# Kernel tuning notes

Hardware: AMD Instinct MI355X
Metric: run time of the kernel (lower is better)

The kernel has to match this reference:

```python
import jax, jax.numpy as jnp
import numpy as np

H = 16          # num_heads
LN_EPS = 1e-5   # torch LayerNorm default


def _ln(x, g, b):
    m = jnp.mean(x, axis=-1, keepdims=True)
    v = jnp.var(x, axis=-1, keepdims=True)
    return (x - m) * jax.lax.rsqrt(v + LN_EPS) * g + b


def _cross_attn(xq, xkv, wq, wk, wv, wp, bp):
    B, N, C = xq.shape
    d = C // H
    scale = d ** -0.5
    q = (xq @ wq).reshape(B, N, H, d).transpose(0, 2, 1, 3)   # bhnd
    k = (xkv @ wk).reshape(B, N, H, d).transpose(0, 2, 1, 3)
    v = (xkv @ wv).reshape(B, N, H, d).transpose(0, 2, 1, 3)
    attn = jax.nn.softmax(jnp.einsum('bhnd,bhmd->bhnm', q, k) * scale, axis=-1)
    out = jnp.einsum('bhnm,bhmd->bhnd', attn, v).transpose(0, 2, 1, 3).reshape(B, N, C)
    return out @ wp + bp


def setup_inputs() -> dict:
    key = jax.random.key(0)
    ks = jax.random.split(key, 16)
    B, N, C, Hid = 8, 1024, 1024, 4096
    s = 0.02
    inp = {
        'x_1': jax.random.normal(ks[0], (B, N, C), jnp.float32),
        'x_2': jax.random.normal(ks[1], (B, N, C), jnp.float32),
        'x_3': jax.random.normal(ks[2], (B, N, C), jnp.float32),
        'ln11_g': jnp.ones((C,), jnp.float32), 'ln11_b': jnp.zeros((C,), jnp.float32),
        'ln12_g': jnp.ones((C,), jnp.float32), 'ln12_b': jnp.zeros((C,), jnp.float32),
        'ln21_g': jnp.ones((C,), jnp.float32), 'ln21_b': jnp.zeros((C,), jnp.float32),
        'ln23_g': jnp.ones((C,), jnp.float32), 'ln23_b': jnp.zeros((C,), jnp.float32),
        'ln2_g': jnp.ones((C,), jnp.float32), 'ln2_b': jnp.zeros((C,), jnp.float32),
        'a1_wq': s * jax.random.normal(ks[3], (C, C), jnp.float32),
        'a1_wk': s * jax.random.normal(ks[4], (C, C), jnp.float32),
        'a1_wv': s * jax.random.normal(ks[5], (C, C), jnp.float32),
        'a1_wp': s * jax.random.normal(ks[6], (C, C), jnp.float32),
        'a1_bp': jnp.zeros((C,), jnp.float32),
        'a2_wq': s * jax.random.normal(ks[7], (C, C), jnp.float32),
        'a2_wk': s * jax.random.normal(ks[8], (C, C), jnp.float32),
        'a2_wv': s * jax.random.normal(ks[9], (C, C), jnp.float32),
        'a2_wp': s * jax.random.normal(ks[10], (C, C), jnp.float32),
        'a2_bp': jnp.zeros((C,), jnp.float32),
        'fc1_w': s * jax.random.normal(ks[11], (C, Hid), jnp.float32),
        'fc1_b': jnp.zeros((Hid,), jnp.float32),
        'fc2_w': s * jax.random.normal(ks[12], (Hid, C), jnp.float32),
        'fc2_b': jnp.zeros((C,), jnp.float32),
    }
    return inp


def reference(x_1, x_2, x_3,
              ln11_g, ln11_b, ln12_g, ln12_b, ln21_g, ln21_b, ln23_g, ln23_b,
              ln2_g, ln2_b,
              a1_wq, a1_wk, a1_wv, a1_wp, a1_bp,
              a2_wq, a2_wk, a2_wv, a2_wp, a2_bp,
              fc1_w, fc1_b, fc2_w, fc2_b):
    # dual cross-attention branches + residual (drop_path/dropout are identity at p=0)
    br1 = _cross_attn(_ln(x_1, ln11_g, ln11_b), _ln(x_2, ln12_g, ln12_b),
                      a1_wq, a1_wk, a1_wv, a1_wp, a1_bp)
    br2 = _cross_attn(_ln(x_1, ln21_g, ln21_b), _ln(x_3, ln23_g, ln23_b),
                      a2_wq, a2_wk, a2_wv, a2_wp, a2_bp)
    x = x_1 + br1 + br2
    # MLP block
    h = jax.nn.gelu(_ln(x, ln2_g, ln2_b) @ fc1_w + fc1_b, approximate=False)
    x = x + (h @ fc2_w + fc2_b)
    return x
```

## Files before the change

### kernel.cpp

```cpp
#include <hip/hip_runtime.h>
#include <hip/hip_bf16.h>
#include <cstdint>

typedef unsigned short u16;
typedef __bf16 v8bf __attribute__((ext_vector_type(8)));
typedef short v4s __attribute__((ext_vector_type(4)));
typedef float v4f __attribute__((ext_vector_type(4)));

__device__ __forceinline__ u16 f2bf(float f) {
  union { float f; uint32_t u; } v; v.f = f;
  return (u16)((v.u + 0x7fffu + ((v.u >> 16) & 1u)) >> 16);
}

#define GLL16(gsrc, ldst) \
  __builtin_amdgcn_global_load_lds((__attribute__((address_space(1))) void*)(gsrc), \
      (__attribute__((address_space(3))) void*)(ldst), 16, 0, 0)

__global__ __launch_bounds__(256) void ln_kernel(
    const float* __restrict__ x, const float* __restrict__ g, const float* __restrict__ bt,
    u16* __restrict__ out)
{
  int row = blockIdx.x, tid = threadIdx.x;
  const float4* xr = (const float4*)(x + (size_t)row * 1024);
  float4 v = xr[tid];
  float s = v.x + v.y + v.z + v.w;
  float ss = v.x*v.x + v.y*v.y + v.z*v.z + v.w*v.w;
  for (int d = 1; d < 64; d <<= 1) { s += __shfl_xor(s, d); ss += __shfl_xor(ss, d); }
  __shared__ float red[8];
  int wv = tid >> 6, lane = tid & 63;
  if (lane == 0) { red[wv] = s; red[4 + wv] = ss; }
  __syncthreads();
  s  = red[0] + red[1] + red[2] + red[3];
  ss = red[4] + red[5] + red[6] + red[7];
  float mean = s * (1.f/1024.f);
  float var  = ss * (1.f/1024.f) - mean*mean;
  float rs = rsqrtf(var + 1e-5f);
  float4 gv = ((const float4*)g)[tid];
  float4 bv = ((const float4*)bt)[tid];
  ushort4 o;
  o.x = f2bf((v.x-mean)*rs*gv.x + bv.x);
  o.y = f2bf((v.y-mean)*rs*gv.y + bv.y);
  o.z = f2bf((v.z-mean)*rs*gv.z + bv.z);
  o.w = f2bf((v.w-mean)*rs*gv.w + bv.w);
  ((ushort4*)out)[(size_t)row*256 + tid] = o;
}

__global__ __launch_bounds__(256) void transpose_cast(
    const float* __restrict__ W, u16* __restrict__ WT, int K, int N)
{
  __shared__ float t[32][33];
  int tiles_n = N >> 5;
  int bn = blockIdx.x % tiles_n, bk = blockIdx.x / tiles_n;
  int tx = threadIdx.x & 31, ty = threadIdx.x >> 5;
  #pragma unroll
  for (int j = 0; j < 4; ++j)
    t[ty + j*8][tx] = W[(size_t)(bk*32 + ty + j*8) * N + bn*32 + tx];
  __syncthreads();
  #pragma unroll
  for (int j = 0; j < 4; ++j)
    WT[(size_t)(bn*32 + ty + j*8) * K + bk*32 + tx] = f2bf(t[tx][ty + j*8]);
}

template<int EPI>
__global__ __launch_bounds__(256, 2) void gemm_bf16(
    const u16* __restrict__ A, const u16* __restrict__ Bt, void* __restrict__ Cout,
    const float* __restrict__ bias, const float* __restrict__ r1, const float* __restrict__ r2,
    int M, int N, int K)
{
  int tiles_n = N >> 7;
  int bm = blockIdx.x / tiles_n, bn = blockIdx.x % tiles_n;
  int tid = threadIdx.x, wv = tid >> 6, lane = tid & 63, quad = lane >> 4, lc = lane & 15;
  int wm = wv & 1, wn = wv >> 1;

  __shared__ __align__(16) u16 lds_[16384];
  char* la = (char*)lds_;
  char* lb = (char*)lds_ + 16384;

  v4f acc[4][4] = {};

  for (int kt = 0; kt < K; kt += 64) {
    __syncthreads();
    #pragma unroll
    for (int c0 = 0; c0 < 4; ++c0) {
      int chunk = wv*4 + c0;
      int off = chunk*1024 + lane*16;
      int row = off >> 7;
      int sc  = (off >> 4) & 7;
      int lg  = sc ^ (row & 7);
      const u16* ga = A  + (size_t)(bm*128 + row) * K + kt + lg*8;
      GLL16(ga, la + chunk*1024);
      const u16* gb = Bt + (size_t)(bn*128 + row) * K + kt + lg*8;
      GLL16(gb, lb + chunk*1024);
    }
    __syncthreads();

    #pragma unroll
    for (int kc = 0; kc < 2; ++kc) {
      v8bf af[4], bfr[4];
      #pragma unroll
      for (int r = 0; r < 4; ++r) {
        int row = wm*64 + r*16 + lc;
        int sc = (kc*4 + quad) ^ (row & 7);
        af[r] = *(const v8bf*)(la + row*128 + sc*16);
      }
      #pragma unroll
      for (int c = 0; c < 4; ++c) {
        int row = wn*64 + c*16 + lc;
        int sc = (kc*4 + quad) ^ (row & 7);
        bfr[c] = *(const v8bf*)(lb + row*128 + sc*16);
      }
      #pragma unroll
      for (int r = 0; r < 4; ++r)
        #pragma unroll
        for (int c = 0; c < 4; ++c)
          acc[r][c] = __builtin_amdgcn_mfma_f32_16x16x32_bf16(af[r], bfr[c], acc[r][c], 0, 0, 0);
    }
  }

  #pragma unroll
  for (int r = 0; r < 4; ++r) {
    int grow = bm*128 + wm*64 + r*16 + quad*4;
    #pragma unroll
    for (int c = 0; c < 4; ++c) {
      int gcol = bn*128 + wn*64 + c*16 + lc;
      if (EPI == 5) {
        ushort4 o;
        o.x = f2bf(acc[r][c][0]); o.y = f2bf(acc[r][c][1]);
        o.z = f2bf(acc[r][c][2]); o.w = f2bf(acc[r][c][3]);
        *(ushort4*)((u16*)Cout + (size_t)gcol * M + grow) = o;
        continue;
      }
      float bv = (EPI != 0) ? bias[gcol] : 0.f;
      #pragma unroll
      for (int i = 0; i < 4; ++i) {
        size_t idx = (size_t)(grow + i) * N + gcol;
        float v = acc[r][c][i] + bv;
        if (EPI == 0) {
          ((u16*)Cout)[idx] = f2bf(v);
        } else if (EPI == 1) {
          float ge = 0.5f * v * (1.f + erff(v * 0.70710678118654752f));
          ((u16*)Cout)[idx] = f2bf(ge);
        } else if (EPI == 2) {
          ((float*)Cout)[idx] = v;
        } else if (EPI == 3) {
          ((float*)Cout)[idx] = v + r1[idx] + r2[idx];
        } else {
          ((float*)Cout)[idx] = v + r1[idx];
        }
      }
    }
  }
}

__global__ __launch_bounds__(256, 2) void attn_kernel(
    const u16* __restrict__ Q, const u16* __restrict__ K, const u16* __restrict__ VT,
    u16* __restrict__ O)
{
  int bid = blockIdx.x;
  int qt = bid & 15, h = (bid >> 4) & 15, b = bid >> 8;
  int tid = threadIdx.x, wv = tid >> 6, lane = tid & 63, quad = lane >> 4, lc = lane & 15;

  __shared__ __align__(16) char lds_[32768];
  char* kt_l = lds_;
  char* vt_l = lds_ + 16384;

  const float scale = 0.125f;

  v8bf qf[2];
  {
    int qrow = qt*64 + wv*16 + lc;
    const u16* qp = Q + ((size_t)(b*1024 + qrow) * 1024 + h*64 + quad*8);
    qf[0] = *(const v8bf*)qp;
    qf[1] = *(const v8bf*)(qp + 32);
  }

  float m_i = -1e30f, l_i = 0.f;
  v4f oacc[4] = {};

  for (int it = 0; it < 8; ++it) {
    int kvb = it * 128;
    __syncthreads();
    #pragma unroll
    for (int c0 = 0; c0 < 4; ++c0) {
      int ch = wv*4 + c0;
      int off = ch*1024 + lane*16;
      {
        int row = off >> 7, sc = (off >> 4) & 7, lg = sc ^ (row & 7);
        const u16* g = K + (size_t)(b*1024 + kvb + row) * 1024 + h*64 + lg*8;
        GLL16(g, kt_l + ch*1024);
      }
      {
        int row = off >> 8, sc = (off >> 4) & 15, lg = sc ^ (row & 15);
        const u16* g = VT + (size_t)(h*64 + row) * 8192 + b*1024 + kvb + lg*8;
        GLL16(g, vt_l + ch*1024);
      }
    }
    __syncthreads();

    v4f s[8] = {};
    #pragma unroll
    for (int ct = 0; ct < 8; ++ct) {
      int row = ct*16 + lc;
      #pragma unroll
      for (int kc = 0; kc < 2; ++kc) {
        int sc = (kc*4 + quad) ^ (row & 7);
        v8bf kf = *(const v8bf*)(kt_l + row*128 + sc*16);
        s[ct] = __builtin_amdgcn_mfma_f32_16x16x32_bf16(kf, qf[kc], s[ct], 0, 0, 0);
      }
    }

    float mx = m_i;
    #pragma unroll
    for (int ct = 0; ct < 8; ++ct)
      #pragma unroll
      for (int i = 0; i < 4; ++i) mx = fmaxf(mx, s[ct][i] * scale);
    mx = fmaxf(mx, __shfl_xor(mx, 16));
    mx = fmaxf(mx, __shfl_xor(mx, 32));
    float alpha = __expf(m_i - mx);
    float rs = 0.f;
    #pragma unroll
    for (int ct = 0; ct < 8; ++ct)
      #pragma unroll
      for (int i = 0; i < 4; ++i) {
        float p = __expf(s[ct][i] * scale - mx);
        s[ct][i] = p;
        rs += p;
      }
    rs += __shfl_xor(rs, 16);
    rs += __shfl_xor(rs, 32);
    l_i = l_i * alpha + rs;
    m_i = mx;
    #pragma unroll
    for (int dt = 0; dt < 4; ++dt)
      #pragma unroll
      for (int i = 0; i < 4; ++i) oacc[dt][i] *= alpha;

    #pragma unroll
    for (int ct = 0; ct < 8; ++ct) {
      v4s pfrag;
      #pragma unroll
      for (int i = 0; i < 4; ++i) pfrag[i] = (short)f2bf(s[ct][i]);
      int lg = ct*2 + (quad >> 1);
      int ho = (quad & 1) * 8;
      #pragma unroll
      for (int dt = 0; dt < 4; ++dt) {
        int rowd = dt*16 + lc;
        int sc = lg ^ (rowd & 15);
        v4s vfrag = *(const v4s*)(vt_l + rowd*256 + sc*16 + ho);
        oacc[dt] = __builtin_amdgcn_mfma_f32_16x16x16bf16_1k(vfrag, pfrag, oacc[dt], 0, 0, 0);
      }
    }
  }

  __syncthreads();
  {
    char* base = kt_l + wv*2048;
    float inv = 1.f / l_i;
    #pragma unroll
    for (int dt = 0; dt < 4; ++dt) {
      ushort4 o;
      o.x = f2bf(oacc[dt][0]*inv); o.y = f2bf(oacc[dt][1]*inv);
      o.z = f2bf(oacc[dt][2]*inv); o.w = f2bf(oacc[dt][3]*inv);
      int lg = dt*2 + (quad >> 1);
      int sc = lg ^ (lc & 7);
      *(ushort4*)(base + lc*128 + sc*16 + (quad & 1)*8) = o;
    }
  }
  __syncthreads();
  {
    char* base = kt_l + wv*2048;
    #pragma unroll
    for (int rep = 0; rep < 2; ++rep) {
      int qr = rep*8 + (lane >> 3);
      int ch = lane & 7;
      int sc = ch ^ (qr & 7);
      uint4 d = *(const uint4*)(base + qr*128 + sc*16);
      *(uint4*)(O + (size_t)(b*1024 + qt*64 + wv*16 + qr) * 1024 + h*64 + ch*8) = d;
    }
  }
}

extern "C" void kernel_launch(void* const* d_in, const int* in_sizes, int n_in,
                              void* d_out, int out_size, void* d_ws, size_t ws_size,
                              hipStream_t stream)
{
  const float* x1    = (const float*)d_in[0];
  const float* x2    = (const float*)d_in[1];
  const float* x3    = (const float*)d_in[2];
  const float* ln11g = (const float*)d_in[3];
  const float* ln11b = (const float*)d_in[4];
  const float* ln12g = (const float*)d_in[5];
  const float* ln12b = (const float*)d_in[6];
  const float* ln21g = (const float*)d_in[7];
  const float* ln21b = (const float*)d_in[8];
  const float* ln23g = (const float*)d_in[9];
  const float* ln23b = (const float*)d_in[10];
  const float* ln2g  = (const float*)d_in[11];
  const float* ln2b  = (const float*)d_in[12];
  const float* a1wq  = (const float*)d_in[13];
  const float* a1wk  = (const float*)d_in[14];
  const float* a1wv  = (const float*)d_in[15];
  const float* a1wp  = (const float*)d_in[16];
  const float* a1bp  = (const float*)d_in[17];
  const float* a2wq  = (const float*)d_in[18];
  const float* a2wk  = (const float*)d_in[19];
  const float* a2wv  = (const float*)d_in[20];
  const float* a2wp  = (const float*)d_in[21];
  const float* a2bp  = (const float*)d_in[22];
  const float* fc1w  = (const float*)d_in[23];
  const float* fc1b  = (const float*)d_in[24];
  const float* fc2w  = (const float*)d_in[25];
  const float* fc2b  = (const float*)d_in[26];

  const int M = 8192, C = 1024, HID = 4096;
  char* ws = (char*)d_ws;
  u16* WT = (u16*)ws;
  #define SLOT(i) ((void*)(ws + ((size_t)8 << 20) + (size_t)(i) * ((size_t)16 << 20)))

  dim3 blk(256);
  const int gC  = (M/128) * (C/128);
  const int gH  = (M/128) * (HID/128);
  const int tCC = (C/32) * (C/32);

  ln_kernel<<<M, blk, 0, stream>>>(x1, ln11g, ln11b, (u16*)SLOT(0));
  ln_kernel<<<M, blk, 0, stream>>>(x2, ln12g, ln12b, (u16*)SLOT(1));

  transpose_cast<<<tCC, blk, 0, stream>>>(a1wq, WT, C, C);
  gemm_bf16<0><<<gC, blk, 0, stream>>>((u16*)SLOT(0), WT, SLOT(2), nullptr, nullptr, nullptr, M, C, C);
  transpose_cast<<<tCC, blk, 0, stream>>>(a1wk, WT, C, C);
  gemm_bf16<0><<<gC, blk, 0, stream>>>((u16*)SLOT(1), WT, SLOT(3), nullptr, nullptr, nullptr, M, C, C);
  transpose_cast<<<tCC, blk, 0, stream>>>(a1wv, WT, C, C);
  gemm_bf16<5><<<gC, blk, 0, stream>>>((u16*)SLOT(1), WT, SLOT(4), nullptr, nullptr, nullptr, M, C, C);

  attn_kernel<<<2048, blk, 0, stream>>>((u16*)SLOT(2), (u16*)SLOT(3), (u16*)SLOT(4), (u16*)SLOT(0));

  transpose_cast<<<tCC, blk, 0, stream>>>(a1wp, WT, C, C);
  gemm_bf16<2><<<gC, blk, 0, stream>>>((u16*)SLOT(0), WT, SLOT(5), a1bp, nullptr, nullptr, M, C, C);

  ln_kernel<<<M, blk, 0, stream>>>(x1, ln21g, ln21b, (u16*)SLOT(1));
  ln_kernel<<<M, blk, 0, stream>>>(x3, ln23g, ln23b, (u16*)SLOT(2));

  transpose_cast<<<tCC, blk, 0, stream>>>(a2wq, WT, C, C);
  gemm_bf16<0><<<gC, blk, 0, stream>>>((u16*)SLOT(1), WT, SLOT(3), nullptr, nullptr, nullptr, M, C, C);
  transpose_cast<<<tCC, blk, 0, stream>>>(a2wk, WT, C, C);
  gemm_bf16<0><<<gC, blk, 0, stream>>>((u16*)SLOT(2), WT, SLOT(4), nullptr, nullptr, nullptr, M, C, C);
  transpose_cast<<<tCC, blk, 0, stream>>>(a2wv, WT, C, C);
  gemm_bf16<5><<<gC, blk, 0, stream>>>((u16*)SLOT(2), WT, SLOT(0), nullptr, nullptr, nullptr, M, C, C);

  attn_kernel<<<2048, blk, 0, stream>>>((u16*)SLOT(3), (u16*)SLOT(4), (u16*)SLOT(0), (u16*)SLOT(1));

  transpose_cast<<<tCC, blk, 0, stream>>>(a2wp, WT, C, C);
  gemm_bf16<3><<<gC, blk, 0, stream>>>((u16*)SLOT(1), WT, SLOT(2), a2bp, x1, (const float*)SLOT(5), M, C, C);

  ln_kernel<<<M, blk, 0, stream>>>((const float*)SLOT(2), ln2g, ln2b, (u16*)SLOT(4));
  transpose_cast<<<(C/32)*(HID/32), blk, 0, stream>>>(fc1w, WT, C, HID);
  gemm_bf16<1><<<gH, blk, 0, stream>>>((u16*)SLOT(4), WT, SLOT(5), fc1b, nullptr, nullptr, M, HID, C);
  transpose_cast<<<(HID/32)*(C/32), blk, 0, stream>>>(fc2w, WT, HID, C);
  gemm_bf16<4><<<gC, blk, 0, stream>>>((u16*)SLOT(5), WT, d_out, fc2b, (const float*)SLOT(2), nullptr, M, C, HID);
  #undef SLOT
}
```

Before: 772.1 us.

## Batch prep, QKV GEMMs, and co-schedule attention with projection GEMM

```diff
diff --git a/kernel.cpp b/kernel.cpp
--- a/kernel.cpp
+++ b/kernel.cpp
@@ -11,10 +11,116 @@
   union { float f; uint32_t u; } v; v.f = f;
   return (u16)((v.u + 0x7fffu + ((v.u >> 16) & 1u)) >> 16);
 }
+__device__ __forceinline__ float bf2f(u16 u) {
+  union { uint32_t u; float f; } v; v.u = ((uint32_t)u) << 16; return v.f;
+}
 
 #define GLL16(gsrc, ldst) \
   __builtin_amdgcn_global_load_lds((__attribute__((address_space(1))) void*)(gsrc), \
       (__attribute__((address_space(3))) void*)(ldst), 16, 0, 0)
+
+#define TILE_MAP(blk, bm, bn) \
+  int bm = ((blk) & 7) * 8 + (((blk) >> 3) & 7); \
+  int bn = (blk) >> 6;
+
+__device__ __forceinline__ void gemm_core(
+    const u16* __restrict__ A, const u16* __restrict__ Bt, int K,
+    char* la, char* lb, int bm, int bn, int tid, v4f acc[4][4])
+{
+  int wv = tid >> 6, lane = tid & 63, quad = lane >> 4, lc = lane & 15;
+  int wm = wv & 1, wn = wv >> 1;
+  for (int kt = 0; kt < K; kt += 64) {
+    __syncthreads();
+    #pragma unroll
+    for (int c0 = 0; c0 < 4; ++c0) {
+      int chunk = wv*4 + c0;
+      int off = chunk*1024 + lane*16;
+      int row = off >> 7;
+      int sc  = (off >> 4) & 7;
+      int lg  = sc ^ (row & 7);
+      GLL16(A  + (size_t)(bm*128 + row) * K + kt + lg*8, la + chunk*1024);
+      GLL16(Bt + (size_t)(bn*128 + row) * K + kt + lg*8, lb + chunk*1024);
+    }
+    __syncthreads();
+    #pragma unroll
+    for (int kc = 0; kc < 2; ++kc) {
+      v8bf af[4], bfr[4];
+      #pragma unroll
+      for (int r = 0; r < 4; ++r) {
+        int row = wm*64 + r*16 + lc;
+        int sc = (kc*4 + quad) ^ (row & 7);
+        af[r] = *(const v8bf*)(la + row*128 + sc*16);
+      }
+      #pragma unroll
+      for (int c = 0; c < 4; ++c) {
+        int row = wn*64 + c*16 + lc;
+        int sc = (kc*4 + quad) ^ (row & 7);
+        bfr[c] = *(const v8bf*)(lb + row*128 + sc*16);
+      }
+      #pragma unroll
+      for (int r = 0; r < 4; ++r)
+        #pragma unroll
+        for (int c = 0; c < 4; ++c)
+          acc[r][c] = __builtin_amdgcn_mfma_f32_16x16x32_bf16(af[r], bfr[c], acc[r][c], 0, 0, 0);
+    }
+  }
+}
+
+struct TDesc { const float* W; u16* WT; int K, N, tstart; };
+struct PrepArgs {
+  TDesc d[10];
+  const float* lx[4]; const float* lg[4]; const float* lb_[4]; u16* lo[4];
+  int ts;
+};
+__global__ __launch_bounds__(256) void prep_kernel(PrepArgs P)
+{
+  __shared__ float sh[32*33];
+  int tid = threadIdx.x;
+  if ((int)blockIdx.x < P.ts) {
+    int bi = blockIdx.x;
+    int idx = 0;
+    #pragma unroll
+    for (int i = 1; i < 10; ++i) if (bi >= P.d[i].tstart) idx = i;
+    const float* W = P.d[idx].W;
+    u16* WT = P.d[idx].WT;
+    int K = P.d[idx].K, N = P.d[idx].N;
+    int loc = bi - P.d[idx].tstart;
+    int tiles_n = N >> 5;
+    int bn = loc % tiles_n, bk = loc / tiles_n;
+    int tx = tid & 31, ty = tid >> 5;
+    #pragma unroll
+    for (int j = 0; j < 4; ++j)
+      sh[(ty + j*8)*33 + tx] = W[(size_t)(bk*32 + ty + j*8) * N + bn*32 + tx];
+    __syncthreads();
+    #pragma unroll
+    for (int j = 0; j < 4; ++j)
+      WT[(size_t)(bn*32 + ty + j*8) * K + bk*32 + tx] = f2bf(sh[tx*33 + ty + j*8]);
+  } else {
+    int lid = blockIdx.x - P.ts;
+    int id = lid >> 13, row = lid & 8191;
+    const float4* xr = (const float4*)(P.lx[id] + (size_t)row * 1024);
+    float4 v = xr[tid];
+    float s = v.x + v.y + v.z + v.w;
+    float ss = v.x*v.x + v.y*v.y + v.z*v.z + v.w*v.w;
+    for (int d = 1; d < 64; d <<= 1) { s += __shfl_xor(s, d); ss += __shfl_xor(ss, d); }
+    int wv = tid >> 6, lane = tid & 63;
+    if (lane == 0) { sh[wv] = s; sh[4 + wv] = ss; }
+    __syncthreads();
+    s  = sh[0] + sh[1] + sh[2] + sh[3];
+    ss = sh[4] + sh[5] + sh[6] + sh[7];
+    float mean = s * (1.f/1024.f);
+    float var  = ss * (1.f/1024.f) - mean*mean;
+    float rs = rsqrtf(var + 1e-5f);
+    float4 gv = ((const float4*)P.lg[id])[tid];
+    float4 bv = ((const float4*)P.lb_[id])[tid];
+    ushort4 o;
+    o.x = f2bf((v.x-mean)*rs*gv.x + bv.x);
+    o.y = f2bf((v.y-mean)*rs*gv.y + bv.y);
+    o.z = f2bf((v.z-mean)*rs*gv.z + bv.z);
+    o.w = f2bf((v.w-mean)*rs*gv.w + bv.w);
+    ((ushort4*)P.lo[id])[(size_t)row*256 + tid] = o;
+  }
+}
 
 __global__ __launch_bounds__(256) void ln_kernel(
     const float* __restrict__ x, const float* __restrict__ g, const float* __restrict__ bt,
@@ -45,125 +151,47 @@
   ((ushort4*)out)[(size_t)row*256 + tid] = o;
 }
 
-__global__ __launch_bounds__(256) void transpose_cast(
-    const float* __restrict__ W, u16* __restrict__ WT, int K, int N)
-{
-  __shared__ float t[32][33];
-  int tiles_n = N >> 5;
-  int bn = blockIdx.x % tiles_n, bk = blockIdx.x / tiles_n;
-  int tx = threadIdx.x & 31, ty = threadIdx.x >> 5;
-  #pragma unroll
-  for (int j = 0; j < 4; ++j)
-    t[ty + j*8][tx] = W[(size_t)(bk*32 + ty + j*8) * N + bn*32 + tx];
-  __syncthreads();
-  #pragma unroll
-  for (int j = 0; j < 4; ++j)
-    WT[(size_t)(bn*32 + ty + j*8) * K + bk*32 + tx] = f2bf(t[tx][ty + j*8]);
-}
-
-template<int EPI>
-__global__ __launch_bounds__(256, 2) void gemm_bf16(
-    const u16* __restrict__ A, const u16* __restrict__ Bt, void* __restrict__ Cout,
-    const float* __restrict__ bias, const float* __restrict__ r1, const float* __restrict__ r2,
-    int M, int N, int K)
-{
-  int tiles_n = N >> 7;
-  int bm = blockIdx.x / tiles_n, bn = blockIdx.x % tiles_n;
+struct QkvArgs { const u16* A[3]; const u16* Bt[3]; u16* C[3]; };
+__global__ __launch_bounds__(256, 3) void gemm_qkv(QkvArgs P)
+{
+  int sub = blockIdx.x >> 9;
+  int local = blockIdx.x & 511;
+  TILE_MAP(local, bm, bn)
   int tid = threadIdx.x, wv = tid >> 6, lane = tid & 63, quad = lane >> 4, lc = lane & 15;
   int wm = wv & 1, wn = wv >> 1;
-
-  __shared__ __align__(16) u16 lds_[16384];
-  char* la = (char*)lds_;
-  char* lb = (char*)lds_ + 16384;
-
+  __shared__ __align__(16) char lds_[32768];
   v4f acc[4][4] = {};
-
-  for (int kt = 0; kt < K; kt += 64) {
-    __syncthreads();
-    #pragma unroll
-    for (int c0 = 0; c0 < 4; ++c0) {
-      int chunk = wv*4 + c0;
-      int off = chunk*1024 + lane*16;
-      int row = off >> 7;
-      int sc  = (off >> 4) & 7;
-      int lg  = sc ^ (row & 7);
-      const u16* ga = A  + (size_t)(bm*128 + row) * K + kt + lg*8;
-      GLL16(ga, la + chunk*1024);
-      const u16* gb = Bt + (size_t)(bn*128 + row) * K + kt + lg*8;
-      GLL16(gb, lb + chunk*1024);
-    }
-    __syncthreads();
-
-    #pragma unroll
-    for (int kc = 0; kc < 2; ++kc) {
-      v8bf af[4], bfr[4];
-      #pragma unroll
-      for (int r = 0; r < 4; ++r) {
-        int row = wm*64 + r*16 + lc;
-        int sc = (kc*4 + quad) ^ (row & 7);
-        af[r] = *(const v8bf*)(la + row*128 + sc*16);
-      }
-      #pragma unroll
-      for (int c = 0; c < 4; ++c) {
-        int row = wn*64 + c*16 + lc;
-        int sc = (kc*4 + quad) ^ (row & 7);
-        bfr[c] = *(const v8bf*)(lb + row*128 + sc*16);
-      }
-      #pragma unroll
-      for (int r = 0; r < 4; ++r)
-        #pragma unroll
-        for (int c = 0; c < 4; ++c)
-          acc[r][c] = __builtin_amdgcn_mfma_f32_16x16x32_bf16(af[r], bfr[c], acc[r][c], 0, 0, 0);
-    }
-  }
-
+  gemm_core(P.A[sub], P.Bt[sub], 1024, lds_, lds_ + 16384, bm, bn, tid, acc);
+
+  u16* Cout = P.C[sub];
   #pragma unroll
   for (int r = 0; r < 4; ++r) {
     int grow = bm*128 + wm*64 + r*16 + quad*4;
     #pragma unroll
     for (int c = 0; c < 4; ++c) {
       int gcol = bn*128 + wn*64 + c*16 + lc;
-      if (EPI == 5) {
+      if (sub == 2) {
         ushort4 o;
         o.x = f2bf(acc[r][c][0]); o.y = f2bf(acc[r][c][1]);
         o.z = f2bf(acc[r][c][2]); o.w = f2bf(acc[r][c][3]);
-        *(ushort4*)((u16*)Cout + (size_t)gcol * M + grow) = o;
-        continue;
-      }
-      float bv = (EPI != 0) ? bias[gcol] : 0.f;
-      #pragma unroll
-      for (int i = 0; i < 4; ++i) {
-        size_t idx = (size_t)(grow + i) * N + gcol;
-        float v = acc[r][c][i] + bv;
-        if (EPI == 0) {
-          ((u16*)Cout)[idx] = f2bf(v);
-        } else if (EPI == 1) {
-          float ge = 0.5f * v * (1.f + erff(v * 0.70710678118654752f));
-          ((u16*)Cout)[idx] = f2bf(ge);
-        } else if (EPI == 2) {
-          ((float*)Cout)[idx] = v;
-        } else if (EPI == 3) {
-          ((float*)Cout)[idx] = v + r1[idx] + r2[idx];
-        } else {
-          ((float*)Cout)[idx] = v + r1[idx];
-        }
-      }
-    }
-  }
-}
-
-__global__ __launch_bounds__(256, 2) void attn_kernel(
+        *(ushort4*)(Cout + (size_t)gcol * 8192 + grow) = o;
+      } else {
+        #pragma unroll
+        for (int i = 0; i < 4; ++i)
+          Cout[(size_t)(grow + i) * 1024 + gcol] = f2bf(acc[r][c][i]);
+      }
+    }
+  }
+}
+
+__device__ __forceinline__ void attn_body(
     const u16* __restrict__ Q, const u16* __restrict__ K, const u16* __restrict__ VT,
-    u16* __restrict__ O)
-{
-  int bid = blockIdx.x;
+    u16* __restrict__ O, int bid, int tid, char* lds_)
+{
   int qt = bid & 15, h = (bid >> 4) & 15, b = bid >> 8;
-  int tid = threadIdx.x, wv = tid >> 6, lane = tid & 63, quad = lane >> 4, lc = lane & 15;
-
-  __shared__ __align__(16) char lds_[32768];
+  int wv = tid >> 6, lane = tid & 63, quad = lane >> 4, lc = lane & 15;
   char* kt_l = lds_;
   char* vt_l = lds_ + 16384;
-
   const float scale = 0.125f;
 
   v8bf qf[2];
@@ -186,13 +214,11 @@
       int off = ch*1024 + lane*16;
       {
         int row = off >> 7, sc = (off >> 4) & 7, lg = sc ^ (row & 7);
-        const u16* g = K + (size_t)(b*1024 + kvb + row) * 1024 + h*64 + lg*8;
-        GLL16(g, kt_l + ch*1024);
+        GLL16(K + (size_t)(b*1024 + kvb + row) * 1024 + h*64 + lg*8, kt_l + ch*1024);
       }
       {
         int row = off >> 8, sc = (off >> 4) & 15, lg = sc ^ (row & 15);
-        const u16* g = VT + (size_t)(h*64 + row) * 8192 + b*1024 + kvb + lg*8;
-        GLL16(g, vt_l + ch*1024);
+        GLL16(VT + (size_t)(h*64 + row) * 8192 + b*1024 + kvb + lg*8, vt_l + ch*1024);
       }
     }
     __syncthreads();
@@ -276,6 +302,127 @@
       int sc = ch ^ (qr & 7);
       uint4 d = *(const uint4*)(base + qr*128 + sc*16);
       *(uint4*)(O + (size_t)(b*1024 + qt*64 + wv*16 + qr) * 1024 + h*64 + ch*8) = d;
+    }
+  }
+}
+
+__global__ __launch_bounds__(256, 4) void attn_kernel(
+    const u16* __restrict__ Q, const u16* __restrict__ K, const u16* __restrict__ VT,
+    u16* __restrict__ O)
+{
+  __shared__ __align__(16) char lds_[32768];
+  attn_body(Q, K, VT, O, blockIdx.x, threadIdx.x, lds_);
+}
+
+__global__ __launch_bounds__(256, 3) void attn_proj_kernel(
+    const u16* __restrict__ Q, const u16* __restrict__ K, const u16* __restrict__ VT,
+    u16* __restrict__ O,
+    const u16* __restrict__ GA, const u16* __restrict__ GBt,
+    const float* __restrict__ Gbias, u16* __restrict__ GC)
+{
+  __shared__ __align__(16) char lds_[32768];
+  int tid = threadIdx.x;
+  if ((int)blockIdx.x < 2048) {
+    attn_body(Q, K, VT, O, blockIdx.x, tid, lds_);
+  } else {
+    int local = blockIdx.x - 2048;
+    TILE_MAP(local, bm, bn)
+    int wv = tid >> 6, lane = tid & 63, quad = lane >> 4, lc = lane & 15;
+    int wm = wv & 1, wn = wv >> 1;
+    v4f acc[4][4] = {};
+    gemm_core(GA, GBt, 1024, lds_, lds_ + 16384, bm, bn, tid, acc);
+    #pragma unroll
+    for (int r = 0; r < 4; ++r) {
+      int grow = bm*128 + wm*64 + r*16 + quad*4;
+      #pragma unroll
+      for (int c = 0; c < 4; ++c) {
+        int gcol = bn*128 + wn*64 + c*16 + lc;
+        float bv = Gbias[gcol];
+        #pragma unroll
+        for (int i = 0; i < 4; ++i)
+          GC[(size_t)(grow + i) * 1024 + gcol] = f2bf(acc[r][c][i] + bv);
+      }
+    }
+  }
+}
+
+__global__ __launch_bounds__(256, 3) void gemm_projadd(
+    const u16* __restrict__ A, const u16* __restrict__ Bt,
+    const float* __restrict__ bias, const float* __restrict__ x1,
+    const u16* __restrict__ o1b, float* __restrict__ xsum)
+{
+  TILE_MAP((int)blockIdx.x, bm, bn)
+  int tid = threadIdx.x, wv = tid >> 6, lane = tid & 63, quad = lane >> 4, lc = lane & 15;
+  int wm = wv & 1, wn = wv >> 1;
+  __shared__ __align__(16) char lds_[32768];
+  v4f acc[4][4] = {};
+  gemm_core(A, Bt, 1024, lds_, lds_ + 16384, bm, bn, tid, acc);
+  #pragma unroll
+  for (int r = 0; r < 4; ++r) {
+    int grow = bm*128 + wm*64 + r*16 + quad*4;
+    #pragma unroll
+    for (int c = 0; c < 4; ++c) {
+      int gcol = bn*128 + wn*64 + c*16 + lc;
+      float bv = bias[gcol];
+      #pragma unroll
+      for (int i = 0; i < 4; ++i) {
+        size_t idx = (size_t)(grow + i) * 1024 + gcol;
+        xsum[idx] = acc[r][c][i] + bv + x1[idx] + bf2f(o1b[idx]);
+      }
+    }
+  }
+}
+
+__global__ __launch_bounds__(256, 3) void gemm_fc1(
+    const u16* __restrict__ A, const u16* __restrict__ Bt,
+    const float* __restrict__ bias, u16* __restrict__ C)
+{
+  TILE_MAP((int)blockIdx.x, bm, bn)
+  int tid = threadIdx.x, wv = tid >> 6, lane = tid & 63, quad = lane >> 4, lc = lane & 15;
+  int wm = wv & 1, wn = wv >> 1;
+  __shared__ __align__(16) char lds_[32768];
+  v4f acc[4][4] = {};
+  gemm_core(A, Bt, 1024, lds_, lds_ + 16384, bm, bn, tid, acc);
+  #pragma unroll
+  for (int r = 0; r < 4; ++r) {
+    int grow = bm*128 + wm*64 + r*16 + quad*4;
+    #pragma unroll
+    for (int c = 0; c < 4; ++c) {
+      int gcol = bn*128 + wn*64 + c*16 + lc;
+      float bv = bias[gcol];
+      #pragma unroll
+      for (int i = 0; i < 4; ++i) {
+        float v = acc[r][c][i] + bv;
+        float ge = 0.5f * v * (1.f + erff(v * 0.70710678118654752f));
+        C[(size_t)(grow + i) * 4096 + gcol] = f2bf(ge);
+      }
+    }
+  }
+}
+
+__global__ __launch_bounds__(256, 3) void gemm_fc2(
+    const u16* __restrict__ A, const u16* __restrict__ Bt,
+    const float* __restrict__ bias, const float* __restrict__ r1,
+    float* __restrict__ C)
+{
+  TILE_MAP((int)blockIdx.x, bm, bn)
+  int tid = threadIdx.x, wv = tid >> 6, lane = tid & 63, quad = lane >> 4, lc = lane & 15;
+  int wm = wv & 1, wn = wv >> 1;
+  __shared__ __align__(16) char lds_[32768];
+  v4f acc[4][4] = {};
+  gemm_core(A, Bt, 4096, lds_, lds_ + 16384, bm, bn, tid, acc);
+  #pragma unroll
+  for (int r = 0; r < 4; ++r) {
+    int grow = bm*128 + wm*64 + r*16 + quad*4;
+    #pragma unroll
+    for (int c = 0; c < 4; ++c) {
+      int gcol = bn*128 + wn*64 + c*16 + lc;
+      float bv = bias[gcol];
+      #pragma unroll
+      for (int i = 0; i < 4; ++i) {
+        size_t idx = (size_t)(grow + i) * 1024 + gcol;
+        C[idx] = acc[r][c][i] + bv + r1[idx];
+      }
     }
   }
 }
@@ -312,50 +459,64 @@
   const float* fc2w  = (const float*)d_in[25];
   const float* fc2b  = (const float*)d_in[26];
 
-  const int M = 8192, C = 1024, HID = 4096;
   char* ws = (char*)d_ws;
-  u16* WT = (u16*)ws;
-  #define SLOT(i) ((void*)(ws + ((size_t)8 << 20) + (size_t)(i) * ((size_t)16 << 20)))
+  const size_t MB = (size_t)1 << 20;
+  u16* wtq1 = (u16*)(ws + 0*MB);  u16* wtk1 = (u16*)(ws + 2*MB);
+  u16* wtv1 = (u16*)(ws + 4*MB);  u16* wtp1 = (u16*)(ws + 6*MB);
+  u16* wtq2 = (u16*)(ws + 8*MB);  u16* wtk2 = (u16*)(ws + 10*MB);
+  u16* wtv2 = (u16*)(ws + 12*MB); u16* wtp2 = (u16*)(ws + 14*MB);
+  u16* wtf1 = (u16*)(ws + 16*MB); u16* wtf2 = (u16*)(ws + 24*MB);
+  u16* xq1  = (u16*)(ws + 32*MB); u16* xkv1 = (u16*)(ws + 48*MB);
+  u16* xq2  = (u16*)(ws + 64*MB); u16* xkv2 = (u16*)(ws + 80*MB);
+  u16* Qb   = (u16*)(ws + 96*MB); u16* Kb   = (u16*)(ws + 112*MB);
+  u16* VTb  = (u16*)(ws + 128*MB);
+  u16* O1   = (u16*)(ws + 32*MB);
+  u16* O2   = (u16*)(ws + 48*MB);
+  u16* o1b  = (u16*)(ws + 64*MB);
+  float* xsum = (float*)(ws + 112*MB);
+  u16* ln2o = (u16*)(ws + 32*MB);
+  u16* hbuf = (u16*)(ws + 48*MB);
 
   dim3 blk(256);
-  const int gC  = (M/128) * (C/128);
-  const int gH  = (M/128) * (HID/128);
-  const int tCC = (C/32) * (C/32);
-
-  ln_kernel<<<M, blk, 0, stream>>>(x1, ln11g, ln11b, (u16*)SLOT(0));
-  ln_kernel<<<M, blk, 0, stream>>>(x2, ln12g, ln12b, (u16*)SLOT(1));
-
-  transpose_cast<<<tCC, blk, 0, stream>>>(a1wq, WT, C, C);
-  gemm_bf16<0><<<gC, blk, 0, stream>>>((u16*)SLOT(0), WT, SLOT(2), nullptr, nullptr, nullptr, M, C, C);
-  transpose_cast<<<tCC, blk, 0, stream>>>(a1wk, WT, C, C);
-  gemm_bf16<0><<<gC, blk, 0, stream>>>((u16*)SLOT(1), WT, SLOT(3), nullptr, nullptr, nullptr, M, C, C);
-  transpose_cast<<<tCC, blk, 0, stream>>>(a1wv, WT, C, C);
-  gemm_bf16<5><<<gC, blk, 0, stream>>>((u16*)SLOT(1), WT, SLOT(4), nullptr, nullptr, nullptr, M, C, C);
-
-  attn_kernel<<<2048, blk, 0, stream>>>((u16*)SLOT(2), (u16*)SLOT(3), (u16*)SLOT(4), (u16*)SLOT(0));
-
-  transpose_cast<<<tCC, blk, 0, stream>>>(a1wp, WT, C, C);
-  gemm_bf16<2><<<gC, blk, 0, stream>>>((u16*)SLOT(0), WT, SLOT(5), a1bp, nullptr, nullptr, M, C, C);
-
-  ln_kernel<<<M, blk, 0, stream>>>(x1, ln21g, ln21b, (u16*)SLOT(1));
-  ln_kernel<<<M, blk, 0, stream>>>(x3, ln23g, ln23b, (u16*)SLOT(2));
-
-  transpose_cast<<<tCC, blk, 0, stream>>>(a2wq, WT, C, C);
-  gemm_bf16<0><<<gC, blk, 0, stream>>>((u16*)SLOT(1), WT, SLOT(3), nullptr, nullptr, nullptr, M, C, C);
-  transpose_cast<<<tCC, blk, 0, stream>>>(a2wk, WT, C, C);
-  gemm_bf16<0><<<gC, blk, 0, stream>>>((u16*)SLOT(2), WT, SLOT(4), nullptr, nullptr, nullptr, M, C, C);
-  transpose_cast<<<tCC, blk, 0, stream>>>(a2wv, WT, C, C);
-  gemm_bf16<5><<<gC, blk, 0, stream>>>((u16*)SLOT(2), WT, SLOT(0), nullptr, nullptr, nullptr, M, C, C);
-
-  attn_kernel<<<2048, blk, 0, stream>>>((u16*)SLOT(3), (u16*)SLOT(4), (u16*)SLOT(0), (u16*)SLOT(1));
-
-  transpose_cast<<<tCC, blk, 0, stream>>>(a2wp, WT, C, C);
-  gemm_bf16<3><<<gC, blk, 0, stream>>>((u16*)SLOT(1), WT, SLOT(2), a2bp, x1, (const float*)SLOT(5), M, C, C);
-
-  ln_kernel<<<M, blk, 0, stream>>>((const float*)SLOT(2), ln2g, ln2b, (u16*)SLOT(4));
-  transpose_cast<<<(C/32)*(HID/32), blk, 0, stream>>>(fc1w, WT, C, HID);
-  gemm_bf16<1><<<gH, blk, 0, stream>>>((u16*)SLOT(4), WT, SLOT(5), fc1b, nullptr, nullptr, M, HID, C);
-  transpose_cast<<<(HID/32)*(C/32), blk, 0, stream>>>(fc2w, WT, HID, C);
-  gemm_bf16<4><<<gC, blk, 0, stream>>>((u16*)SLOT(5), WT, d_out, fc2b, (const float*)SLOT(2), nullptr, M, C, HID);
-  #undef SLOT
-}
+
+  PrepArgs pa;
+  const float* Ws[10]  = {a1wq, a1wk, a1wv, a1wp, a2wq, a2wk, a2wv, a2wp, fc1w, fc2w};
+  u16* WTs[10]         = {wtq1, wtk1, wtv1, wtp1, wtq2, wtk2, wtv2, wtp2, wtf1, wtf2};
+  int Kd[10] = {1024,1024,1024,1024,1024,1024,1024,1024,1024,4096};
+  int Nd[10] = {1024,1024,1024,1024,1024,1024,1024,1024,4096,1024};
+  int ts = 0;
+  for (int i = 0; i < 10; ++i) {
+    pa.d[i] = {Ws[i], WTs[i], Kd[i], Nd[i], ts};
+    ts += (Kd[i]/32) * (Nd[i]/32);
+  }
+  pa.ts = ts;
+  pa.lx[0]=x1; pa.lg[0]=ln11g; pa.lb_[0]=ln11b; pa.lo[0]=xq1;
+  pa.lx[1]=x2; pa.lg[1]=ln12g; pa.lb_[1]=ln12b; pa.lo[1]=xkv1;
+  pa.lx[2]=x1; pa.lg[2]=ln21g; pa.lb_[2]=ln21b; pa.lo[2]=xq2;
+  pa.lx[3]=x3; pa.lg[3]=ln23g; pa.lb_[3]=ln23b; pa.lo[3]=xkv2;
+  prep_kernel<<<ts + 32768, blk, 0, stream>>>(pa);
+
+  QkvArgs g1;
+  g1.A[0]=xq1;  g1.Bt[0]=wtq1; g1.C[0]=Qb;
+  g1.A[1]=xkv1; g1.Bt[1]=wtk1; g1.C[1]=Kb;
+  g1.A[2]=xkv1; g1.Bt[2]=wtv1; g1.C[2]=VTb;
+  gemm_qkv<<<1536, blk, 0, stream>>>(g1);
+
+  attn_kernel<<<2048, blk, 0, stream>>>(Qb, Kb, VTb, O1);
+
+  QkvArgs g2;
+  g2.A[0]=xq2;  g2.Bt[0]=wtq2; g2.C[0]=Qb;
+  g2.A[1]=xkv2; g2.Bt[1]=wtk2; g2.C[1]=Kb;
+  g2.A[2]=xkv2; g2.Bt[2]=wtv2; g2.C[2]=VTb;
+  gemm_qkv<<<1536, blk, 0, stream>>>(g2);
+
+  attn_proj_kernel<<<2048 + 512, blk, 0, stream>>>(Qb, Kb, VTb, O2, O1, wtp1, a1bp, o1b);
+
+  gemm_projadd<<<512, blk, 0, stream>>>(O2, wtp2, a2bp, x1, o1b, xsum);
+
+  ln_kernel<<<8192, blk, 0, stream>>>(xsum, ln2g, ln2b, ln2o);
+
+  gemm_fc1<<<2048, blk, 0, stream>>>(ln2o, wtf1, fc1b, hbuf);
+
+  gemm_fc2<<<512, blk, 0, stream>>>(hbuf, wtf2, fc2b, xsum, (float*)d_out);
+}
```

After: 742.6 us. -3.8%, faster.
